# Performance work log

Hardware: AMD Instinct MI355X
Metric: run time of the kernel (lower is better)

The kernel has to match this reference:

```python
import jax, jax.numpy as jnp
import numpy as np

B, C, H, W = 8, 256, 64, 64
IC = 128  # inter_channels = C // reduction


def setup_inputs() -> dict:
    key = jax.random.key(0)
    ks = jax.random.split(key, 9)
    s_in = 1.0 / np.sqrt(C)
    s_ic = 1.0 / np.sqrt(IC)
    return {
        "x": jax.random.normal(ks[0], (B, C, H, W), jnp.float32),
        "wg": jax.random.normal(ks[1], (IC, C), jnp.float32) * s_in,
        "bg": jax.random.normal(ks[2], (IC,), jnp.float32) * s_in,
        "wt": jax.random.normal(ks[3], (IC, C), jnp.float32) * s_in,
        "bt": jax.random.normal(ks[4], (IC,), jnp.float32) * s_in,
        "wp": jax.random.normal(ks[5], (IC, C), jnp.float32) * s_in,
        "bp": jax.random.normal(ks[6], (IC,), jnp.float32) * s_in,
        "wm": jax.random.normal(ks[7], (C, IC), jnp.float32) * s_ic,
        "bm": jax.random.normal(ks[8], (C,), jnp.float32) * s_ic,
    }


def reference(x, wg, bg, wt, bt, wp, bp, wm, bm):
    b, c, h, w = x.shape
    n = h * w
    xf = x.reshape(b, c, n)  # [B, C, N]
    # 1x1 convs are channel matmuls; relu applied after each (as in source)
    g = jax.nn.relu(jnp.einsum('ic,bcn->bni', wg, xf) + bg)          # [B, N, IC]
    theta = jax.nn.relu(jnp.einsum('ic,bcn->bni', wt, xf) + bt)      # [B, N, IC]
    phi = jax.nn.relu(jnp.einsum('ic,bcn->bin', wp, xf) + bp[:, None])  # [B, IC, N]
    scores = jnp.einsum('bni,bim->bnm', theta, phi)                  # [B, N, N] (no scaling)
    attn = jax.nn.softmax(scores, axis=-1)
    out = jnp.einsum('bnm,bmi->bni', attn, g)                        # [B, N, IC]
    mask = jax.nn.relu(jnp.einsum('oc,bnc->bon', wm, out) + bm[None, :, None])
    return mask.reshape(b, c, h, w) + x
```

## Files before the change

kernel.cpp:

```cpp
#include <hip/hip_runtime.h>

typedef __bf16 bf16x8 __attribute__((ext_vector_type(8)));
typedef float f32x4 __attribute__((ext_vector_type(4)));
typedef float f32x16 __attribute__((ext_vector_type(16)));
typedef unsigned short ushort8 __attribute__((ext_vector_type(8)));
typedef unsigned short ushort4v __attribute__((ext_vector_type(4)));
typedef unsigned int uint4v __attribute__((ext_vector_type(4)));

union Frag {
  ushort8 u;
  bf16x8 b;
  uint4v w;
};

__device__ __forceinline__ unsigned short f2bf(float f) {
  unsigned int u = __float_as_uint(f);
  u += 0x7fffu + ((u >> 16) & 1u);
  return (unsigned short)(u >> 16);
}

__device__ __forceinline__ f32x4 fz4() {
  f32x4 v; v[0] = 0.f; v[1] = 0.f; v[2] = 0.f; v[3] = 0.f; return v;
}

__device__ __forceinline__ f32x16 fz16() {
  f32x16 v;
#pragma unroll
  for (int i = 0; i < 16; ++i) v[i] = 0.f;
  return v;
}

#define MFMA16(a, b, c) __builtin_amdgcn_mfma_f32_16x16x32_bf16(a, b, c, 0, 0, 0)
#define MFMA32(a, b, c) __builtin_amdgcn_mfma_f32_32x32x16_bf16(a, b, c, 0, 0, 0)

#define LOG2E 1.4426950408889634f


__global__ void k_prep(const float* __restrict__ wg, const float* __restrict__ wt,
                       const float* __restrict__ wp, const float* __restrict__ wm,
                       unsigned short* __restrict__ wcat, unsigned short* __restrict__ wmb) {
  int t = blockIdx.x * 256 + threadIdx.x;
  if (t < 98304) {
    int o = t >> 8;
    const float* src = (o < 128) ? wt : ((o < 256) ? wp : wg);
    wcat[t] = f2bf(src[(o & 127) * 256 + (t & 255)]);
  }
  if (t < 32768) wmb[t] = f2bf(wm[t]);
}

__device__ __forceinline__ void stage_x(const float* __restrict__ x, int bx, int pt0,
                                        unsigned short* xb, int tid) {
  int c0 = (tid >> 2) * 4;
  int psub = (tid & 3) * 16;
  const float* xbase = x + (size_t)bx * 256 * 4096 + pt0;
  for (int ppc = 0; ppc < 4; ++ppc) {
    int p0 = psub + ppc * 4;
    f32x4 r0 = *(const f32x4*)(xbase + (size_t)(c0 + 0) * 4096 + p0);
    f32x4 r1 = *(const f32x4*)(xbase + (size_t)(c0 + 1) * 4096 + p0);
    f32x4 r2 = *(const f32x4*)(xbase + (size_t)(c0 + 2) * 4096 + p0);
    f32x4 r3 = *(const f32x4*)(xbase + (size_t)(c0 + 3) * 4096 + p0);
    for (int e = 0; e < 4; ++e) {
      ushort4v wv;
      wv[0] = f2bf(r0[e]); wv[1] = f2bf(r1[e]); wv[2] = f2bf(r2[e]); wv[3] = f2bf(r3[e]);
      *(ushort4v*)&xb[(p0 + e) * 264 + c0] = wv;
    }
  }
}

__global__ __launch_bounds__(256, 2) void k_proj(
    const float* __restrict__ x, const unsigned short* __restrict__ wcat,
    const float* __restrict__ bt, const float* __restrict__ bp,
    const float* __restrict__ bg,
    unsigned short* __restrict__ theta, unsigned short* __restrict__ phiS,
    unsigned short* __restrict__ vS) {
  __shared__ unsigned short xb[64 * 264];
  int gb = blockIdx.x >> 6;
  size_t ob_off = (size_t)gb * 524288;
  int pt0 = (blockIdx.x & 63) << 6;
  int tid = threadIdx.x;
  stage_x(x, gb, pt0, xb, tid);
  __syncthreads();
  int l = tid & 63, w = tid >> 6, lr = l & 15, lg = l >> 4;
  int obase = w * 64;
  f32x4 acc[4][4];
  f32x4 accg[8];
  for (int i = 0; i < 4; ++i) for (int j = 0; j < 4; ++j) acc[i][j] = fz4();
  for (int i = 0; i < 8; ++i) accg[i] = fz4();
  for (int kc = 0; kc < 8; ++kc) {
    int ko = kc * 32 + 8 * lg;
    Frag wa[4], xq[4];
    for (int ot = 0; ot < 4; ++ot)
      wa[ot].u = *(const ushort8*)(wcat + (size_t)(obase + ot * 16 + lr) * 256 + ko);
    for (int pt = 0; pt < 4; ++pt)
      xq[pt].u = *(const ushort8*)&xb[(pt * 16 + lr) * 264 + ko];
    for (int ot = 0; ot < 4; ++ot)
      for (int pt = 0; pt < 4; ++pt)
        acc[ot][pt] = MFMA16(wa[ot].b, xq[pt].b, acc[ot][pt]);
    for (int ot = 0; ot < 8; ++ot) {
      Frag wb;
      wb.u = *(const ushort8*)(wcat + (size_t)(256 + ot * 16 + lr) * 256 + ko);
      accg[ot] = MFMA16(xq[w].b, wb.b, accg[ot]);
    }
  }
  for (int ot = 0; ot < 4; ++ot) {
    int o0 = obase + ot * 16 + 4 * lg;
    float bias[4];
    for (int j = 0; j < 4; ++j) bias[j] = (o0 < 128) ? bt[o0 + j] : bp[o0 + j - 128];
    for (int pt = 0; pt < 4; ++pt) {
      int n = pt0 + pt * 16 + lr;
      ushort4v wv;
      if (o0 < 128) {
        for (int j = 0; j < 4; ++j) {
          float v = acc[ot][pt][j] + bias[j];
          wv[j] = f2bf(v > 0.f ? v * LOG2E : 0.f);
        }
        *(ushort4v*)(theta + ob_off + (size_t)n * 128 + o0) = wv;
      } else {
        for (int j = 0; j < 4; ++j) {
          float v = acc[ot][pt][j] + bias[j];
          wv[j] = f2bf(v > 0.f ? v : 0.f);
        }
        int oc = o0 - 128;
        size_t a = (size_t)(n >> 5) * 4096 + (size_t)(oc >> 4) * 512 +
                   (size_t)((oc >> 3) & 1) * 256 + (size_t)(n & 31) * 8 + (oc & 7);
        *(ushort4v*)(phiS + ob_off + a) = wv;
      }
    }
  }
  for (int ot = 0; ot < 8; ++ot) {
    int o = ot * 16 + lr;
    float bias = bg[o];
    int n0 = pt0 + w * 16 + 4 * lg;
    ushort4v wv;
    for (int j = 0; j < 4; ++j) {
      float v = accg[ot][j] + bias;
      wv[j] = f2bf(v > 0.f ? v : 0.f);
    }
    size_t a = (size_t)(n0 >> 5) * 4096 +
               (size_t)((o >> 5) * 2 + ((n0 >> 4) & 1)) * 512 +
               (size_t)((((n0 >> 3) & 1) << 5) | (o & 31)) * 8 + (n0 & 7);
    *(ushort4v*)(vS + ob_off + a) = wv;
  }
}

__global__ __launch_bounds__(256, 2) void k_attn(
    const unsigned short* __restrict__ theta, const unsigned short* __restrict__ phiS,
    const unsigned short* __restrict__ vS, unsigned short* __restrict__ out_nm) {
  __shared__ float osum[64][132];
  __shared__ float mls[4][32][2];
  int bid = blockIdx.x;
  int b = bid & 7;
  int bq0 = (bid >> 3) << 6;
  int tid = threadIdx.x;
  int l = tid & 63, wid = tid >> 6;
  int ml = l & 31, hi = l >> 5;
  int l8 = l * 8;
  int qh = wid & 1, kh = wid >> 1;
  int q0 = bq0 + qh * 32;

  const size_t tbase = ((size_t)b << 12) * 128;
  const unsigned short* pS = phiS + (size_t)b * 524288;
  const unsigned short* vSb = vS + (size_t)b * 524288;

  Frag qf[8];
#pragma unroll
  for (int kc = 0; kc < 8; ++kc)
    qf[kc].u = *(const ushort8*)(theta + tbase +
        (size_t)(q0 + ml) * 128 + kc * 16 + 8 * hi);

  f32x16 oacc[4];
#pragma unroll
  for (int db = 0; db < 4; ++db) oacc[db] = fz16();
  float m = -1e30f, sden = 0.f;

  int t0 = kh * 64;

  Frag pa[8];
#pragma unroll
  for (int kc = 0; kc < 8; ++kc)
    pa[kc].u = *(const ushort8*)(pS + (size_t)t0 * 4096 + kc * 512 + l8);

  for (int kt = 0; kt < 64; ++kt) {
    int t = t0 + kt;

    f32x16 sacc = fz16();
#pragma unroll
    for (int kc = 0; kc < 8; ++kc) sacc = MFMA32(pa[kc].b, qf[kc].b, sacc);

    Frag vt[8];
#pragma unroll
    for (int t8 = 0; t8 < 8; ++t8)
      vt[t8].u = *(const ushort8*)(vSb + (size_t)t * 4096 + t8 * 512 + l8);

#pragma unroll
    for (int kc = 0; kc < 8; ++kc)
      pa[kc].u = *(const ushort8*)(pS + (size_t)(t + 1) * 4096 + kc * 512 + l8);

    float m8[8];
#pragma unroll
    for (int j = 0; j < 8; ++j) m8[j] = fmaxf(sacc[j], sacc[j + 8]);
    float t1 = fmaxf(fmaxf(m8[0], m8[1]), m8[2]);
    float t2 = fmaxf(fmaxf(m8[3], m8[4]), m8[5]);
    float t3 = fmaxf(m8[6], m8[7]);
    float mt = fmaxf(fmaxf(t1, t2), t3);
    mt = fmaxf(mt, __shfl_xor(mt, 32));
    if (!__all(mt <= m + 24.0f)) {
      float mn = fmaxf(m, mt);
      float sc = __builtin_exp2f(m - mn);
      sden *= sc;
#pragma unroll
      for (int db = 0; db < 4; ++db) oacc[db] *= sc;
      m = mn;
    }
    float p[16];
#pragma unroll
    for (int r = 0; r < 16; ++r) p[r] = __builtin_exp2f(sacc[r] - m);
    float s8[8];
#pragma unroll
    for (int j = 0; j < 8; ++j) s8[j] = p[j] + p[j + 8];
    float ps = ((s8[0] + s8[1]) + (s8[2] + s8[3])) + ((s8[4] + s8[5]) + (s8[6] + s8[7]));
    ps += __shfl_xor(ps, 32);
    sden += ps;

    unsigned wpk[8], pw[8];
#pragma unroll
    for (int j = 0; j < 8; ++j) {
      unsigned u0 = __float_as_uint(p[2 * j]);
      unsigned u1 = __float_as_uint(p[2 * j + 1]);
      wpk[j] = (u1 & 0xFFFF0000u) | (u0 >> 16);
    }
#pragma unroll
    for (int j = 0; j < 8; ++j) pw[j] = (unsigned)__shfl_xor((int)wpk[j], 32);
    Frag bf0, bf1;
    bf0.w[0] = hi ? pw[2] : wpk[0];
    bf0.w[1] = hi ? pw[3] : wpk[1];
    bf0.w[2] = hi ? wpk[2] : pw[0];
    bf0.w[3] = hi ? wpk[3] : pw[1];
    bf1.w[0] = hi ? pw[6] : wpk[4];
    bf1.w[1] = hi ? pw[7] : wpk[5];
    bf1.w[2] = hi ? wpk[6] : pw[4];
    bf1.w[3] = hi ? wpk[7] : pw[5];

#pragma unroll
    for (int db = 0; db < 4; ++db) {
      oacc[db] = MFMA32(vt[db * 2].b, bf0.b, oacc[db]);
      oacc[db] = MFMA32(vt[db * 2 + 1].b, bf1.b, oacc[db]);
    }
  }

  if (l < 32) { mls[wid][l][0] = m; mls[wid][l][1] = sden; }
  __syncthreads();
  {
    float M = fmaxf(mls[qh][ml][0], mls[qh + 2][ml][0]);
    float sc = __builtin_exp2f(m - M);
    int orow = qh * 32 + ml;
    if (kh == 0) {
#pragma unroll
      for (int db = 0; db < 4; ++db)
#pragma unroll
        for (int r = 0; r < 16; ++r) {
          int d = db * 32 + (r & 3) + 8 * (r >> 2) + 4 * hi;
          osum[orow][d] = oacc[db][r] * sc;
        }
    }
    __syncthreads();
    if (kh == 1) {
#pragma unroll
      for (int db = 0; db < 4; ++db)
#pragma unroll
        for (int r = 0; r < 16; ++r) {
          int d = db * 32 + (r & 3) + 8 * (r >> 2) + 4 * hi;
          osum[orow][d] += oacc[db][r] * sc;
        }
    }
    __syncthreads();
  }
  {
    int row = tid & 63;
    int mlr = row & 31, qhr = row >> 5;
    int t_ = (bq0 + row) >> 5;
    float Mx = fmaxf(mls[qhr][mlr][0], mls[qhr + 2][mlr][0]);
    float Lt = mls[qhr][mlr][1] * __builtin_exp2f(mls[qhr][mlr][0] - Mx) +
               mls[qhr + 2][mlr][1] * __builtin_exp2f(mls[qhr + 2][mlr][0] - Mx);
    float inv = 1.0f / Lt;
#pragma unroll
    for (int u = 0; u < 2; ++u) {
      int d0 = (wid + 4 * u) * 16;
      ushort8 w1;
      for (int k = 0; k < 8; ++k) w1[k] = f2bf(osum[row][d0 + k] * inv);
      ushort8 w2;
      for (int k = 0; k < 8; ++k) w2[k] = f2bf(osum[row][d0 + 8 + k] * inv);
      size_t a = (size_t)b * 524288 + (size_t)t_ * 4096 +
                 (size_t)(d0 >> 4) * 512 + (size_t)mlr * 8;
      *(ushort8*)(out_nm + a) = w1;
      *(ushort8*)(out_nm + a + 256) = w2;
    }
  }
}

__global__ __launch_bounds__(256, 2) void k_mask(
    const unsigned short* __restrict__ wmb, const unsigned short* __restrict__ out_nm,
    const float* __restrict__ bm, const float* __restrict__ x,
    float* __restrict__ out) {
  int gb = blockIdx.x >> 6;
  size_t boff = (size_t)gb * 524288;
  int n0 = (blockIdx.x & 63) << 6;
  int tid = threadIdx.x;
  int l = tid & 63, w = tid >> 6, lr = l & 15, lg = l >> 4;
  int ob = w * 64;
  f32x4 acc[4][4];
  for (int i = 0; i < 4; ++i) for (int j = 0; j < 4; ++j) acc[i][j] = fz4();
  for (int kc = 0; kc < 4; ++kc) {
    int ko = kc * 32 + 8 * lg;
    int kc2 = kc * 2 + (lg >> 1), hi2 = lg & 1;
    Frag wa[4], xq[4];
    for (int ot = 0; ot < 4; ++ot)
      wa[ot].u = *(const ushort8*)(wmb + (size_t)(ob + ot * 16 + lr) * 128 + ko);
    for (int nt = 0; nt < 4; ++nt) {
      int t = (n0 >> 5) + (nt >> 1);
      int mln = ((nt & 1) << 4) + lr;
      xq[nt].u = *(const ushort8*)(out_nm + boff + (size_t)t * 4096 +
                                   (size_t)kc2 * 512 + (size_t)(hi2 * 32 + mln) * 8);
    }
    for (int ot = 0; ot < 4; ++ot)
      for (int nt = 0; nt < 4; ++nt)
        acc[ot][nt] = MFMA16(wa[ot].b, xq[nt].b, acc[ot][nt]);
  }
  for (int ot = 0; ot < 4; ++ot) {
    int o0 = ob + ot * 16 + 4 * lg;
    for (int nt = 0; nt < 4; ++nt) {
      int n = n0 + nt * 16 + lr;
      for (int j = 0; j < 4; ++j) {
        size_t idx = ((size_t)(gb << 8) + o0 + j) * 4096 + n;
        float v = acc[ot][nt][j] + bm[o0 + j];
        v = v > 0.f ? v : 0.f;
        out[idx] = v + x[idx];
      }
    }
  }
}

extern "C" void kernel_launch(void* const* d_in, const int* in_sizes, int n_in,
                              void* d_out, int out_size, void* d_ws, size_t ws_size,
                              hipStream_t stream) {
  const float* x  = (const float*)d_in[0];
  const float* wg = (const float*)d_in[1];
  const float* bg = (const float*)d_in[2];
  const float* wt = (const float*)d_in[3];
  const float* bt = (const float*)d_in[4];
  const float* wp = (const float*)d_in[5];
  const float* bp = (const float*)d_in[6];
  const float* wm = (const float*)d_in[7];
  const float* bm = (const float*)d_in[8];
  float* out = (float*)d_out;

  const size_t SLAB = 524288;
  unsigned short* wcat  = (unsigned short*)d_ws;
  unsigned short* wmb   = wcat + 98304;
  unsigned short* theta = wmb + 32768;
  unsigned short* phiS  = theta + 8 * SLAB;
  unsigned short* vS    = phiS + 8 * SLAB;

  k_prep<<<384, 256, 0, stream>>>(wg, wt, wp, wm, wcat, wmb);
  k_proj<<<512, 256, 0, stream>>>(x, wcat, bt, bp, bg, theta, phiS, vS);
  k_attn<<<512, 256, 0, stream>>>(theta, phiS, vS, theta );
  k_mask<<<512, 256, 0, stream>>>(wmb, theta, bm, x, out);
}
```

Baseline: 163.5 us.

## Stage phi and V tiles through double-buffered LDS via global_load_lds in attention

The attention kernel now loads each key tile's phi and V fragments with direct global-to-LDS loads into a double-buffered shared staging area. Each of the four waves fetches one of the four tiles, then all waves read their fragments from LDS. Before, the two query-half waves each loaded the same tiles from global memory, so the aim is to halve redundant global/L2 traffic and overlap the next tile's fetch with compute. In exchange it adds a block-wide barrier every iteration and LDS read traffic. The osum reduction buffer is aliased onto the staging area to keep shared memory use in check.

```diff
diff --git a/kernel.cpp b/kernel.cpp
--- a/kernel.cpp
+++ b/kernel.cpp
@@ -34,6 +34,11 @@
 #define MFMA32(a, b, c) __builtin_amdgcn_mfma_f32_32x32x16_bf16(a, b, c, 0, 0, 0)
 
 #define LOG2E 1.4426950408889634f
+
+#define GLD_LDS16(gsrc, ldst)                                                     \
+  __builtin_amdgcn_global_load_lds(                                               \
+      (const __attribute__((address_space(1))) unsigned int*)(const void*)(gsrc), \
+      (__attribute__((address_space(3))) unsigned int*)(void*)(ldst), 16, 0, 0)
 
 
 __global__ void k_prep(const float* __restrict__ wg, const float* __restrict__ wt,
@@ -146,8 +151,10 @@
 __global__ __launch_bounds__(256, 2) void k_attn(
     const unsigned short* __restrict__ theta, const unsigned short* __restrict__ phiS,
     const unsigned short* __restrict__ vS, unsigned short* __restrict__ out_nm) {
-  __shared__ float osum[64][132];
+  __shared__ unsigned short sstage[2][4][4096];
   __shared__ float mls[4][32][2];
+  float* osum = (float*)&sstage[0][0][0];
+
   int bid = blockIdx.x;
   int b = bid & 7;
   int bq0 = (bid >> 3) << 6;
@@ -162,6 +169,9 @@
   const unsigned short* pS = phiS + (size_t)b * 524288;
   const unsigned short* vSb = vS + (size_t)b * 524288;
 
+  const unsigned short* sbase = (wid < 2) ? pS : vSb;
+  int skh = wid & 1;
+
   Frag qf[8];
 #pragma unroll
   for (int kc = 0; kc < 8; ++kc)
@@ -173,15 +183,33 @@
   for (int db = 0; db < 4; ++db) oacc[db] = fz16();
   float m = -1e30f, sden = 0.f;
 
-  int t0 = kh * 64;
-
-  Frag pa[8];
-#pragma unroll
-  for (int kc = 0; kc < 8; ++kc)
-    pa[kc].u = *(const ushort8*)(pS + (size_t)t0 * 4096 + kc * 512 + l8);
-
+  {
+    const unsigned short* src = sbase + (size_t)(skh * 64) * 4096;
+    unsigned short* dst = &sstage[0][wid][0];
+#pragma unroll
+    for (int i = 0; i < 8; ++i)
+      GLD_LDS16(src + i * 512 + l8, dst + i * 512);
+  }
+  __syncthreads();
+
+  int cur = 0;
   for (int kt = 0; kt < 64; ++kt) {
-    int t = t0 + kt;
+    {
+      int ktn = (kt + 1) & 63;
+      const unsigned short* src = sbase + (size_t)(skh * 64 + ktn) * 4096;
+      unsigned short* dst = &sstage[cur ^ 1][wid][0];
+#pragma unroll
+      for (int i = 0; i < 8; ++i)
+        GLD_LDS16(src + i * 512 + l8, dst + i * 512);
+    }
+
+    const unsigned short* php = &sstage[cur][kh][0];
+    const unsigned short* vvp = &sstage[cur][2 + kh][0];
+
+    Frag pa[8];
+#pragma unroll
+    for (int kc = 0; kc < 8; ++kc)
+      pa[kc].u = *(const ushort8*)(php + kc * 512 + l8);
 
     f32x16 sacc = fz16();
 #pragma unroll
@@ -190,11 +218,7 @@
     Frag vt[8];
 #pragma unroll
     for (int t8 = 0; t8 < 8; ++t8)
-      vt[t8].u = *(const ushort8*)(vSb + (size_t)t * 4096 + t8 * 512 + l8);
-
-#pragma unroll
-    for (int kc = 0; kc < 8; ++kc)
-      pa[kc].u = *(const ushort8*)(pS + (size_t)(t + 1) * 4096 + kc * 512 + l8);
+      vt[t8].u = *(const ushort8*)(vvp + t8 * 512 + l8);
 
     float m8[8];
 #pragma unroll
@@ -246,6 +270,9 @@
       oacc[db] = MFMA32(vt[db * 2].b, bf0.b, oacc[db]);
       oacc[db] = MFMA32(vt[db * 2 + 1].b, bf1.b, oacc[db]);
     }
+
+    __syncthreads();
+    cur ^= 1;
   }
 
   if (l < 32) { mls[wid][l][0] = m; mls[wid][l][1] = sden; }
@@ -260,7 +287,7 @@
 #pragma unroll
         for (int r = 0; r < 16; ++r) {
           int d = db * 32 + (r & 3) + 8 * (r >> 2) + 4 * hi;
-          osum[orow][d] = oacc[db][r] * sc;
+          osum[orow * 132 + d] = oacc[db][r] * sc;
         }
     }
     __syncthreads();
@@ -270,7 +297,7 @@
 #pragma unroll
         for (int r = 0; r < 16; ++r) {
           int d = db * 32 + (r & 3) + 8 * (r >> 2) + 4 * hi;
-          osum[orow][d] += oacc[db][r] * sc;
+          osum[orow * 132 + d] += oacc[db][r] * sc;
         }
     }
     __syncthreads();
@@ -287,9 +314,9 @@
     for (int u = 0; u < 2; ++u) {
       int d0 = (wid + 4 * u) * 16;
       ushort8 w1;
-      for (int k = 0; k < 8; ++k) w1[k] = f2bf(osum[row][d0 + k] * inv);
+      for (int k = 0; k < 8; ++k) w1[k] = f2bf(osum[row * 132 + d0 + k] * inv);
       ushort8 w2;
-      for (int k = 0; k < 8; ++k) w2[k] = f2bf(osum[row][d0 + 8 + k] * inv);
+      for (int k = 0; k < 8; ++k) w2[k] = f2bf(osum[row * 132 + d0 + 8 + k] * inv);
       size_t a = (size_t)b * 524288 + (size_t)t_ * 4096 +
                  (size_t)(d0 >> 4) * 512 + (size_t)mlr * 8;
       *(ushort8*)(out_nm + a) = w1;
```

Result: slower. 167.1 us (+2.2%).
